# Kernel optimization log

Hardware: AMD Instinct MI355X
Metric: run time of the kernel (lower is better)

## Reference

```python
import jax, jax.numpy as jnp
import numpy as np

EPS = 1e-6

def rmsnorm(x, scale):
    return x * jax.lax.rsqrt(jnp.mean(x * x, axis=-1, keepdims=True) + EPS) * scale

def setup_inputs() -> dict:
    key = jax.random.key(0)
    ks = jax.random.split(key, 8)
    B1, B2 = 16, 64
    D, H, A = 8192, 1024, 2          # deter_size, hidden_size, action_size
    S, C, G = 32, 64, 8              # stoch_size, classes, blocks
    sc = 0.02                        # trunc-normal-ish init scale
    f32 = jnp.float32
    return dict(
        deter=jax.random.normal(ks[0], (B1, B2, D), f32),
        stoch=jax.random.normal(ks[1], (B1, B2, S, C), f32),
        action=jax.random.normal(ks[2], (B1, B2, A), f32),
        W1=(jax.random.normal(ks[3], (H, D), f32) * sc),
        b1=jnp.zeros((H,), f32),
        s1=jnp.ones((H,), f32),
        W2=(jax.random.normal(ks[4], (H, S * C), f32) * sc),
        b2=jnp.zeros((H,), f32),
        s2=jnp.ones((H,), f32),
        W3=(jax.random.normal(ks[5], (H, A), f32) * sc),
        b3=jnp.zeros((H,), f32),
        s3=jnp.ones((H,), f32),
        Wb1=(jax.random.normal(ks[6], (G, (3 * G * H + D) // G, D // G), f32) * sc),
        bb1=jnp.zeros((D,), f32),
        sb1=jnp.ones((D,), f32),
        Wb2=(jax.random.normal(ks[7], (G, D // G, 3 * D // G), f32) * sc),
        bb2=jnp.zeros((3 * D,), f32),
    )

def reference(deter, stoch, action, W1, b1, s1, W2, b2, s2, W3, b3, s3, Wb1, bb1, sb1, Wb2, bb2):
    batch_shape = deter.shape[:-1]
    D = deter.shape[-1]
    d = deter.reshape(-1, D)                       # (B, D)
    B = d.shape[0]
    G = Wb1.shape[0]
    H = W1.shape[0]
    s = stoch.reshape(B, -1)                       # (B, S*C)
    a = action.reshape(B, -1)                      # (B, A)
    a = a / jax.lax.stop_gradient(jnp.maximum(1.0, jnp.abs(a)))
    # three parallel Linear + RMSNorm + SiLU branches
    x1 = jax.nn.silu(rmsnorm(d @ W1.T + b1, s1))
    x2 = jax.nn.silu(rmsnorm(s @ W2.T + b2, s2))
    x3 = jax.nn.silu(rmsnorm(a @ W3.T + b3, s3))
    x = jnp.concatenate([x1, x2, x3], axis=-1)     # (B, 3H)
    x = jnp.broadcast_to(x[:, None, :], (B, G, 3 * H))
    x = jnp.concatenate([x, d.reshape(B, G, D // G)], axis=-1)  # (B, G, 3H + D/G)
    # block-diagonal grouped GEMM + RMSNorm + SiLU (dyn_layers=1)
    h = jnp.einsum('bgi,gio->bgo', x, Wb1).reshape(B, D) + bb1
    h = jax.nn.silu(rmsnorm(h, sb1))
    # final block-diagonal GEMM -> 3*D gate pre-activations
    y = jnp.einsum('bgi,gio->bgo', h.reshape(B, G, D // G), Wb2).reshape(B, 3 * D) + bb2
    r, c, u = jnp.split(y.reshape(B, G, -1), 3, axis=-1)        # each (B, G, D/G)
    reset = jax.nn.sigmoid(r.reshape(B, D))
    cand = jnp.tanh(reset * c.reshape(B, D))
    update = jax.nn.sigmoid(u.reshape(B, D) - 1.0)
    next_deter = update * cand + (1.0 - update) * d
    return next_deter.reshape(*batch_shape, D)
```

## Files before the change

### kernel.cpp

```cpp
#include <hip/hip_runtime.h>
#include <stdint.h>

typedef unsigned short ushort_t;
typedef __attribute__((ext_vector_type(8))) short bf16x8;
typedef __attribute__((ext_vector_type(4))) float f32x4;

#define EPS 1e-6f

__device__ __forceinline__ float b2f(ushort_t u) {
    union { uint32_t i; float f; } v; v.i = ((uint32_t)u) << 16; return v.f;
}
__device__ __forceinline__ ushort_t f2b(float f) {
    union { float f; uint32_t i; } v; v.f = f;
    uint32_t x = v.i;
    uint32_t r = (x + 0x7fffu + ((x >> 16) & 1u)) >> 16;
    return (ushort_t)r;
}

__device__ __forceinline__ void async_copy16(const void* g, void* l) {
    __builtin_amdgcn_global_load_lds(
        (const __attribute__((address_space(1))) uint32_t*)(uintptr_t)g,
        (__attribute__((address_space(3))) uint32_t*)(uintptr_t)l,
        16, 0, 0);
}

__global__ __launch_bounds__(256) void cast_f32_bf16_k(const float* __restrict__ src,
                                                       ushort_t* __restrict__ dst, int n4) {
    int i = blockIdx.x * 256 + threadIdx.x;
    if (i >= n4) return;
    float4 v = ((const float4*)src)[i];
    ushort4 o;
    o.x = f2b(v.x); o.y = f2b(v.y); o.z = f2b(v.z); o.w = f2b(v.w);
    ((ushort4*)dst)[i] = o;
}

__global__ __launch_bounds__(256) void zero_f32_k(float* __restrict__ dst, int n4) {
    int i = blockIdx.x * 256 + threadIdx.x;
    if (i >= n4) return;
    ((float4*)dst)[i] = make_float4(0.f, 0.f, 0.f, 0.f);
}

__global__ __launch_bounds__(256) void transpose_cast_k(const float* __restrict__ src,
                                                        ushort_t* __restrict__ dst,
                                                        int R, int C) {
    __shared__ float tile[32][33];
    int bat = blockIdx.z;
    int c0 = blockIdx.x * 32, r0 = blockIdx.y * 32;
    const float* s = src + (size_t)bat * R * C;
    ushort_t* d = dst + (size_t)bat * R * C;
    int tx = threadIdx.x, ty = threadIdx.y;
    float4 v = *(const float4*)&s[(size_t)(r0 + ty) * C + c0 + tx * 4];
    tile[ty][tx * 4 + 0] = v.x;
    tile[ty][tx * 4 + 1] = v.y;
    tile[ty][tx * 4 + 2] = v.z;
    tile[ty][tx * 4 + 3] = v.w;
    __syncthreads();
    ushort4 o;
    o.x = f2b(tile[tx * 4 + 0][ty]);
    o.y = f2b(tile[tx * 4 + 1][ty]);
    o.z = f2b(tile[tx * 4 + 2][ty]);
    o.w = f2b(tile[tx * 4 + 3][ty]);
    *(ushort4*)&d[(size_t)(c0 + ty) * R + r0 + tx * 4] = o;
}

template <int MODE, bool OUT_BF16, bool ATOMIC>
__global__ __launch_bounds__(256) void gemm_bt_k(
    const ushort_t* __restrict__ Aa, const ushort_t* __restrict__ Ab,
    const ushort_t* __restrict__ Bw,
    float* __restrict__ Cf, ushort_t* __restrict__ Cb,
    int lda, int ldb, int ldc, int Ksl, int k0base) {
    __shared__ __align__(16) ushort_t As[2][128 * 64];
    __shared__ __align__(16) ushort_t Bs[2][128 * 64];
    const int tid = threadIdx.x;

    const int nxy = gridDim.x * gridDim.y;
    const int flat = blockIdx.x + (blockIdx.y << 3);
    const int cpx = nxy >> 3;
    const int L = (flat & 7) * cpx + (flat >> 3);
    const int bm = L & 7, bn = L >> 3;
    const int bz = blockIdx.z;
    const int k0 = k0base + bz * Ksl;
    const int m0 = bm * 128, n0 = bn * 128;
    const int lane = tid & 63, w = tid >> 6;
    const int wm = (w & 1) * 64, wn = (w >> 1) * 64;

    f32x4 acc[4][4];
#pragma unroll
    for (int i = 0; i < 4; i++)
#pragma unroll
        for (int j = 0; j < 4; j++) acc[i][j] = (f32x4){0.f, 0.f, 0.f, 0.f};

    auto a_ptr = [&](int m, int kk) -> const ushort_t* {
        if (MODE == 0) {
            return Aa + (size_t)m * lda + kk;
        } else if (MODE == 1) {
            if (kk < 3072) return Aa + (size_t)m * 3072 + kk;
            int g = n0 >> 10;
            return Ab + (size_t)m * 8192 + g * 1024 + (kk - 3072);
        } else {
            int g = n0 / 3072;
            return Aa + (size_t)m * 8192 + g * 1024 + kk;
        }
    };

    const int srow = tid >> 3;
    const int sslot = tid & 7;
    const int gco = (sslot ^ (srow & 7)) << 3;
    const int lco = sslot << 3;

    auto stage = [&](int buf, int kk) {
#pragma unroll
        for (int p = 0; p < 4; ++p) {
            int r = (p << 5) + srow;
            async_copy16(a_ptr(m0 + r, kk + gco), &As[buf][r * 64 + lco]);
            async_copy16(Bw + (size_t)(n0 + r) * ldb + kk + gco, &Bs[buf][r * 64 + lco]);
        }
    };

    const int nt = Ksl >> 6;
    stage(0, k0);
    __syncthreads();

    const int qc = lane >> 4;
    const int rl = lane & 15;
    int cur = 0;

    for (int t = 0; t < nt; ++t) {
        if (t + 1 < nt) stage(cur ^ 1, k0 + ((t + 1) << 6));

#pragma unroll
        for (int h = 0; h < 2; ++h) {
            bf16x8 af[4], bfr[4];
#pragma unroll
            for (int i = 0; i < 4; i++) {
                int ra = wm + i * 16 + rl;
                int slot = ((h << 2) + qc) ^ (ra & 7);
                af[i] = *(const bf16x8*)&As[cur][ra * 64 + (slot << 3)];
            }
#pragma unroll
            for (int j = 0; j < 4; j++) {
                int rb = wn + j * 16 + rl;
                int slot = ((h << 2) + qc) ^ (rb & 7);
                bfr[j] = *(const bf16x8*)&Bs[cur][rb * 64 + (slot << 3)];
            }
#pragma unroll
            for (int i = 0; i < 4; i++)
#pragma unroll
                for (int j = 0; j < 4; j++)
                    acc[i][j] = __builtin_amdgcn_mfma_f32_16x16x32_bf16(af[i], bfr[j], acc[i][j], 0, 0, 0);
        }

        if (t + 1 < nt) {
            __syncthreads();
            cur ^= 1;
        }
    }

    const int cr = (lane >> 4) * 4, cc = lane & 15;
#pragma unroll
    for (int i = 0; i < 4; i++) {
#pragma unroll
        for (int j = 0; j < 4; j++) {
#pragma unroll
            for (int r = 0; r < 4; r++) {
                int row = m0 + wm + i * 16 + cr + r;
                int col = n0 + wn + j * 16 + cc;
                float v = acc[i][j][r];
                if (ATOMIC) {
                    atomicAdd(&Cf[(size_t)row * ldc + col], v);
                } else if (OUT_BF16) {
                    Cb[(size_t)row * ldc + col] = f2b(v);
                } else {
                    Cf[(size_t)row * ldc + col] = v;
                }
            }
        }
    }
}

__global__ __launch_bounds__(256) void branch3_k(const float* __restrict__ act,
                                                 const float* __restrict__ W3,
                                                 float* __restrict__ xpre) {
    int idx = blockIdx.x * 256 + threadIdx.x;
    int b = idx >> 10, h = idx & 1023;
    float a0 = act[b * 2 + 0], a1 = act[b * 2 + 1];
    a0 = a0 / fmaxf(1.f, fabsf(a0));
    a1 = a1 / fmaxf(1.f, fabsf(a1));
    float v = a0 * W3[h * 2 + 0] + a1 * W3[h * 2 + 1];
    xpre[(size_t)b * 3072 + 2048 + h] = v;
}

__global__ __launch_bounds__(256) void norm_silu_1024_k(
    const float* __restrict__ xpre,
    const float* __restrict__ b1, const float* __restrict__ s1,
    const float* __restrict__ b2, const float* __restrict__ s2,
    const float* __restrict__ b3, const float* __restrict__ s3,
    ushort_t* __restrict__ xbf) {
    int b = blockIdx.x, c = blockIdx.y, tid = threadIdx.x;
    const float* bias = (c == 0) ? b1 : (c == 1) ? b2 : b3;
    const float* scl  = (c == 0) ? s1 : (c == 1) ? s2 : s3;
    const float* src = xpre + (size_t)b * 3072 + c * 1024;
    float4 v = ((const float4*)src)[tid];
    float4 bb = ((const float4*)bias)[tid];
    v.x += bb.x; v.y += bb.y; v.z += bb.z; v.w += bb.w;
    float ss = v.x * v.x + v.y * v.y + v.z * v.z + v.w * v.w;
#pragma unroll
    for (int off = 32; off > 0; off >>= 1) ss += __shfl_down(ss, off, 64);
    __shared__ float wsum[4];
    int lane = tid & 63, wid = tid >> 6;
    if (lane == 0) wsum[wid] = ss;
    __syncthreads();
    float tot = wsum[0] + wsum[1] + wsum[2] + wsum[3];
    float rms = rsqrtf(tot * (1.0f / 1024.0f) + EPS);
    float4 sc = ((const float4*)scl)[tid];
    float o0 = v.x * rms * sc.x; o0 = o0 / (1.f + __expf(-o0));
    float o1 = v.y * rms * sc.y; o1 = o1 / (1.f + __expf(-o1));
    float o2 = v.z * rms * sc.z; o2 = o2 / (1.f + __expf(-o2));
    float o3 = v.w * rms * sc.w; o3 = o3 / (1.f + __expf(-o3));
    ushort4 o; o.x = f2b(o0); o.y = f2b(o1); o.z = f2b(o2); o.w = f2b(o3);
    ((ushort4*)(xbf + (size_t)b * 3072 + c * 1024))[tid] = o;
}

__global__ __launch_bounds__(256) void norm_silu_8192_k(const float* __restrict__ hpre,
                                                        const float* __restrict__ bb1,
                                                        const float* __restrict__ sb1,
                                                        ushort_t* __restrict__ hbf) {
    int b = blockIdx.x, tid = threadIdx.x;
    const float4* src = (const float4*)(hpre + (size_t)b * 8192);
    float4 v[8];
    float ss = 0.f;
#pragma unroll
    for (int k = 0; k < 8; k++) {
        float4 t = src[tid + k * 256];
        float4 bv = ((const float4*)bb1)[tid + k * 256];
        t.x += bv.x; t.y += bv.y; t.z += bv.z; t.w += bv.w;
        v[k] = t;
        ss += t.x * t.x + t.y * t.y + t.z * t.z + t.w * t.w;
    }
#pragma unroll
    for (int off = 32; off > 0; off >>= 1) ss += __shfl_down(ss, off, 64);
    __shared__ float wsum[4];
    int lane = tid & 63, wid = tid >> 6;
    if (lane == 0) wsum[wid] = ss;
    __syncthreads();
    float tot = wsum[0] + wsum[1] + wsum[2] + wsum[3];
    float rms = rsqrtf(tot * (1.0f / 8192.0f) + EPS);
    ushort_t* dst = hbf + (size_t)b * 8192;
#pragma unroll
    for (int k = 0; k < 8; k++) {
        float4 sv = ((const float4*)sb1)[tid + k * 256];
        float o0 = v[k].x * rms * sv.x; o0 = o0 / (1.f + __expf(-o0));
        float o1 = v[k].y * rms * sv.y; o1 = o1 / (1.f + __expf(-o1));
        float o2 = v[k].z * rms * sv.z; o2 = o2 / (1.f + __expf(-o2));
        float o3 = v[k].w * rms * sv.w; o3 = o3 / (1.f + __expf(-o3));
        ushort4 o; o.x = f2b(o0); o.y = f2b(o1); o.z = f2b(o2); o.w = f2b(o3);
        ((ushort4*)dst)[tid + k * 256] = o;
    }
}

__global__ __launch_bounds__(256) void gates_k(const ushort_t* __restrict__ y,
                                               const float* __restrict__ bb2,
                                               const float* __restrict__ deter,
                                               float* __restrict__ out) {
    int idx = blockIdx.x * 256 + threadIdx.x;
    int f = idx * 4;
    int b = f >> 13, d = f & 8191;
    int g = d >> 10, j = d & 1023;
    size_t ybase = (size_t)b * 24576 + g * 3072 + j;
    ushort4 rv = *(const ushort4*)(y + ybase);
    ushort4 cv = *(const ushort4*)(y + ybase + 1024);
    ushort4 uv = *(const ushort4*)(y + ybase + 2048);
    float4 bbr = *(const float4*)(bb2 + g * 3072 + j);
    float4 bbc = *(const float4*)(bb2 + g * 3072 + 1024 + j);
    float4 bbu = *(const float4*)(bb2 + g * 3072 + 2048 + j);
    float4 dv = *(const float4*)(deter + f);
    float rr[4] = {b2f(rv.x) + bbr.x, b2f(rv.y) + bbr.y, b2f(rv.z) + bbr.z, b2f(rv.w) + bbr.w};
    float cc[4] = {b2f(cv.x) + bbc.x, b2f(cv.y) + bbc.y, b2f(cv.z) + bbc.z, b2f(cv.w) + bbc.w};
    float uu[4] = {b2f(uv.x) + bbu.x, b2f(uv.y) + bbu.y, b2f(uv.z) + bbu.z, b2f(uv.w) + bbu.w};
    float dd[4] = {dv.x, dv.y, dv.z, dv.w};
    float oo[4];
#pragma unroll
    for (int t = 0; t < 4; t++) {
        float reset = 1.f / (1.f + __expf(-rr[t]));
        float cand = tanhf(reset * cc[t]);
        float upd = 1.f / (1.f + __expf(-(uu[t] - 1.f)));
        oo[t] = upd * cand + (1.f - upd) * dd[t];
    }
    float4 o; o.x = oo[0]; o.y = oo[1]; o.z = oo[2]; o.w = oo[3];
    *(float4*)(out + f) = o;
}

extern "C" void kernel_launch(void* const* d_in, const int* in_sizes, int n_in,
                              void* d_out, int out_size, void* d_ws, size_t ws_size,
                              hipStream_t stream) {
    const float* deter = (const float*)d_in[0];
    const float* stoch = (const float*)d_in[1];
    const float* action = (const float*)d_in[2];
    const float* W1 = (const float*)d_in[3];
    const float* b1 = (const float*)d_in[4];
    const float* s1 = (const float*)d_in[5];
    const float* W2 = (const float*)d_in[6];
    const float* b2 = (const float*)d_in[7];
    const float* s2 = (const float*)d_in[8];
    const float* W3 = (const float*)d_in[9];
    const float* b3 = (const float*)d_in[10];
    const float* s3 = (const float*)d_in[11];
    const float* Wb1 = (const float*)d_in[12];
    const float* bb1 = (const float*)d_in[13];
    const float* sb1 = (const float*)d_in[14];
    const float* Wb2 = (const float*)d_in[15];
    const float* bb2 = (const float*)d_in[16];
    float* out = (float*)d_out;

    char* ws = (char*)d_ws;
    ushort_t* dbf  = (ushort_t*)(ws + 0);
    ushort_t* sbf  = (ushort_t*)(ws + 16777216);
    ushort_t* W1bf = (ushort_t*)(ws + 20971520);
    ushort_t* W2bf = (ushort_t*)(ws + 37748736);
    ushort_t* Wb1T = (ushort_t*)(ws + 41943040);
    ushort_t* Wb2T = (ushort_t*)(ws + 109051904);
    float*    xpre = (float*)   (ws + 159383552);
    ushort_t* xbf  = (ushort_t*)(ws + 171966464);
    float*    hpre = (float*)   (ws + 178257920);
    ushort_t* hbf  = (ushort_t*)(ws + 211812352);
    ushort_t* ybf  = (ushort_t*)(ws + 228589568);

    cast_f32_bf16_k<<<8192, 256, 0, stream>>>(deter, dbf, 2097152);
    cast_f32_bf16_k<<<2048, 256, 0, stream>>>(stoch, sbf, 524288);
    cast_f32_bf16_k<<<8192, 256, 0, stream>>>(W1, W1bf, 2097152);
    cast_f32_bf16_k<<<2048, 256, 0, stream>>>(W2, W2bf, 524288);
    transpose_cast_k<<<dim3(32, 128, 8), dim3(8, 32), 0, stream>>>(Wb1, Wb1T, 4096, 1024);
    transpose_cast_k<<<dim3(96, 32, 8), dim3(8, 32), 0, stream>>>(Wb2, Wb2T, 1024, 3072);
    zero_f32_k<<<3072, 256, 0, stream>>>(xpre, 786432);

    gemm_bt_k<0, false, true><<<dim3(8, 8, 4), 256, 0, stream>>>(
        dbf, nullptr, W1bf, xpre, nullptr, 8192, 8192, 3072, 2048, 0);
    gemm_bt_k<0, false, true><<<dim3(8, 8, 2), 256, 0, stream>>>(
        sbf, nullptr, W2bf, xpre + 1024, nullptr, 2048, 2048, 3072, 1024, 0);
    branch3_k<<<4096, 256, 0, stream>>>(action, W3, xpre);

    norm_silu_1024_k<<<dim3(1024, 3), 256, 0, stream>>>(xpre, b1, s1, b2, s2, b3, s3, xbf);

    gemm_bt_k<1, false, false><<<dim3(8, 64, 1), 256, 0, stream>>>(
        xbf, dbf, Wb1T, hpre, nullptr, 0, 4096, 8192, 4096, 0);

    norm_silu_8192_k<<<1024, 256, 0, stream>>>(hpre, bb1, sb1, hbf);

    gemm_bt_k<2, true, false><<<dim3(8, 192, 1), 256, 0, stream>>>(
        hbf, nullptr, Wb2T, nullptr, ybf, 0, 1024, 24576, 1024, 0);

    gates_k<<<8192, 256, 0, stream>>>(ybf, bb2, deter, out);
}
```

Baseline: 634.0 us.

## Replace split-K atomics with partial buffers, fuse casts, and relax GEMM pipeline waits

The split-K GEMMs now write each K-slice to a separate region of a wider partial buffer instead of using atomicAdd. The norm kernel sums those partials, so the zeroing kernel and atomic contention go away. The four cast launches are merged into one kernel. The GEMM main loop swaps __syncthreads for explicit vmcnt waits plus s_barrier, so the next tile's async loads can stay in flight during compute. The partial buffer reuses the hpre workspace region, and the hand-written waitcnt counts must match the number of issued loads exactly.

```diff
diff --git a/kernel.cpp b/kernel.cpp
--- a/kernel.cpp
+++ b/kernel.cpp
@@ -24,20 +24,21 @@
         16, 0, 0);
 }
 
-__global__ __launch_bounds__(256) void cast_f32_bf16_k(const float* __restrict__ src,
-                                                       ushort_t* __restrict__ dst, int n4) {
-    int i = blockIdx.x * 256 + threadIdx.x;
-    if (i >= n4) return;
-    float4 v = ((const float4*)src)[i];
+__global__ __launch_bounds__(256) void cast4_k(
+    const float* __restrict__ s0, ushort_t* __restrict__ d0, int n0,
+    const float* __restrict__ s1, ushort_t* __restrict__ d1, int n1,
+    const float* __restrict__ s2, ushort_t* __restrict__ d2, int n2,
+    const float* __restrict__ s3, ushort_t* __restrict__ d3) {
+    int j = blockIdx.x * 256 + threadIdx.x;
+    const float* s; ushort_t* d;
+    if (j < n0) { s = s0; d = d0; }
+    else if ((j -= n0) < n1) { s = s1; d = d1; }
+    else if ((j -= n1) < n2) { s = s2; d = d2; }
+    else { j -= n2; s = s3; d = d3; }
+    float4 v = ((const float4*)s)[j];
     ushort4 o;
     o.x = f2b(v.x); o.y = f2b(v.y); o.z = f2b(v.z); o.w = f2b(v.w);
-    ((ushort4*)dst)[i] = o;
-}
-
-__global__ __launch_bounds__(256) void zero_f32_k(float* __restrict__ dst, int n4) {
-    int i = blockIdx.x * 256 + threadIdx.x;
-    if (i >= n4) return;
-    ((float4*)dst)[i] = make_float4(0.f, 0.f, 0.f, 0.f);
+    ((ushort4*)d)[j] = o;
 }
 
 __global__ __launch_bounds__(256) void transpose_cast_k(const float* __restrict__ src,
@@ -63,12 +64,12 @@
     *(ushort4*)&d[(size_t)(c0 + ty) * R + r0 + tx * 4] = o;
 }
 
-template <int MODE, bool OUT_BF16, bool ATOMIC>
+template <int MODE, bool OUT_BF16>
 __global__ __launch_bounds__(256) void gemm_bt_k(
     const ushort_t* __restrict__ Aa, const ushort_t* __restrict__ Ab,
     const ushort_t* __restrict__ Bw,
     float* __restrict__ Cf, ushort_t* __restrict__ Cb,
-    int lda, int ldb, int ldc, int Ksl, int k0base) {
+    int lda, int ldb, int ldc, int Ksl, int k0base, int czoff) {
     __shared__ __align__(16) ushort_t As[2][128 * 64];
     __shared__ __align__(16) ushort_t Bs[2][128 * 64];
     const int tid = threadIdx.x;
@@ -81,6 +82,7 @@
     const int bz = blockIdx.z;
     const int k0 = k0base + bz * Ksl;
     const int m0 = bm * 128, n0 = bn * 128;
+    const int cz = bz * czoff;
     const int lane = tid & 63, w = tid >> 6;
     const int wm = (w & 1) * 64, wn = (w >> 1) * 64;
 
@@ -119,14 +121,21 @@
 
     const int nt = Ksl >> 6;
     stage(0, k0);
-    __syncthreads();
+    __builtin_amdgcn_sched_barrier(0);
 
     const int qc = lane >> 4;
     const int rl = lane & 15;
     int cur = 0;
 
     for (int t = 0; t < nt; ++t) {
-        if (t + 1 < nt) stage(cur ^ 1, k0 + ((t + 1) << 6));
+        if (t + 1 < nt) {
+            stage(cur ^ 1, k0 + ((t + 1) << 6));
+            asm volatile("s_waitcnt vmcnt(8)" ::: "memory");
+        } else {
+            asm volatile("s_waitcnt vmcnt(0)" ::: "memory");
+        }
+        __builtin_amdgcn_s_barrier();
+        __builtin_amdgcn_sched_barrier(0);
 
 #pragma unroll
         for (int h = 0; h < 2; ++h) {
@@ -151,7 +160,9 @@
         }
 
         if (t + 1 < nt) {
-            __syncthreads();
+            __builtin_amdgcn_sched_barrier(0);
+            __builtin_amdgcn_s_barrier();
+            __builtin_amdgcn_sched_barrier(0);
             cur ^= 1;
         }
     }
@@ -164,11 +175,9 @@
 #pragma unroll
             for (int r = 0; r < 4; r++) {
                 int row = m0 + wm + i * 16 + cr + r;
-                int col = n0 + wn + j * 16 + cc;
+                int col = n0 + cz + wn + j * 16 + cc;
                 float v = acc[i][j][r];
-                if (ATOMIC) {
-                    atomicAdd(&Cf[(size_t)row * ldc + col], v);
-                } else if (OUT_BF16) {
+                if (OUT_BF16) {
                     Cb[(size_t)row * ldc + col] = f2b(v);
                 } else {
                     Cf[(size_t)row * ldc + col] = v;
@@ -180,18 +189,18 @@
 
 __global__ __launch_bounds__(256) void branch3_k(const float* __restrict__ act,
                                                  const float* __restrict__ W3,
-                                                 float* __restrict__ xpre) {
+                                                 float* __restrict__ xacc) {
     int idx = blockIdx.x * 256 + threadIdx.x;
     int b = idx >> 10, h = idx & 1023;
     float a0 = act[b * 2 + 0], a1 = act[b * 2 + 1];
     a0 = a0 / fmaxf(1.f, fabsf(a0));
     a1 = a1 / fmaxf(1.f, fabsf(a1));
     float v = a0 * W3[h * 2 + 0] + a1 * W3[h * 2 + 1];
-    xpre[(size_t)b * 3072 + 2048 + h] = v;
+    xacc[(size_t)b * 7168 + 6144 + h] = v;
 }
 
 __global__ __launch_bounds__(256) void norm_silu_1024_k(
-    const float* __restrict__ xpre,
+    const float* __restrict__ xacc,
     const float* __restrict__ b1, const float* __restrict__ s1,
     const float* __restrict__ b2, const float* __restrict__ s2,
     const float* __restrict__ b3, const float* __restrict__ s3,
@@ -199,8 +208,14 @@
     int b = blockIdx.x, c = blockIdx.y, tid = threadIdx.x;
     const float* bias = (c == 0) ? b1 : (c == 1) ? b2 : b3;
     const float* scl  = (c == 0) ? s1 : (c == 1) ? s2 : s3;
-    const float* src = xpre + (size_t)b * 3072 + c * 1024;
-    float4 v = ((const float4*)src)[tid];
+    const float* row = xacc + (size_t)b * 7168 + ((c == 0) ? 0 : (c == 1) ? 4096 : 6144);
+    const int np = (c == 0) ? 4 : (c == 1) ? 2 : 1;
+    float4 v = ((const float4*)row)[tid];
+#pragma unroll 4
+    for (int p = 1; p < np; ++p) {
+        float4 t = ((const float4*)(row + p * 1024))[tid];
+        v.x += t.x; v.y += t.y; v.z += t.z; v.w += t.w;
+    }
     float4 bb = ((const float4*)bias)[tid];
     v.x += bb.x; v.y += bb.y; v.z += bb.z; v.w += bb.w;
     float ss = v.x * v.x + v.y * v.y + v.z * v.z + v.w * v.w;
@@ -319,35 +334,34 @@
     ushort_t* W2bf = (ushort_t*)(ws + 37748736);
     ushort_t* Wb1T = (ushort_t*)(ws + 41943040);
     ushort_t* Wb2T = (ushort_t*)(ws + 109051904);
-    float*    xpre = (float*)   (ws + 159383552);
     ushort_t* xbf  = (ushort_t*)(ws + 171966464);
     float*    hpre = (float*)   (ws + 178257920);
     ushort_t* hbf  = (ushort_t*)(ws + 211812352);
     ushort_t* ybf  = (ushort_t*)(ws + 228589568);
-
-    cast_f32_bf16_k<<<8192, 256, 0, stream>>>(deter, dbf, 2097152);
-    cast_f32_bf16_k<<<2048, 256, 0, stream>>>(stoch, sbf, 524288);
-    cast_f32_bf16_k<<<8192, 256, 0, stream>>>(W1, W1bf, 2097152);
-    cast_f32_bf16_k<<<2048, 256, 0, stream>>>(W2, W2bf, 524288);
+    float*    xacc = hpre;
+
+    cast4_k<<<20480, 256, 0, stream>>>(deter, dbf, 2097152,
+                                       stoch, sbf, 524288,
+                                       W1, W1bf, 2097152,
+                                       W2, W2bf);
     transpose_cast_k<<<dim3(32, 128, 8), dim3(8, 32), 0, stream>>>(Wb1, Wb1T, 4096, 1024);
     transpose_cast_k<<<dim3(96, 32, 8), dim3(8, 32), 0, stream>>>(Wb2, Wb2T, 1024, 3072);
-    zero_f32_k<<<3072, 256, 0, stream>>>(xpre, 786432);
-
-    gemm_bt_k<0, false, true><<<dim3(8, 8, 4), 256, 0, stream>>>(
-        dbf, nullptr, W1bf, xpre, nullptr, 8192, 8192, 3072, 2048, 0);
-    gemm_bt_k<0, false, true><<<dim3(8, 8, 2), 256, 0, stream>>>(
-        sbf, nullptr, W2bf, xpre + 1024, nullptr, 2048, 2048, 3072, 1024, 0);
-    branch3_k<<<4096, 256, 0, stream>>>(action, W3, xpre);
-
-    norm_silu_1024_k<<<dim3(1024, 3), 256, 0, stream>>>(xpre, b1, s1, b2, s2, b3, s3, xbf);
-
-    gemm_bt_k<1, false, false><<<dim3(8, 64, 1), 256, 0, stream>>>(
-        xbf, dbf, Wb1T, hpre, nullptr, 0, 4096, 8192, 4096, 0);
+
+    gemm_bt_k<0, false><<<dim3(8, 8, 4), 256, 0, stream>>>(
+        dbf, nullptr, W1bf, xacc, nullptr, 8192, 8192, 7168, 2048, 0, 1024);
+    gemm_bt_k<0, false><<<dim3(8, 8, 2), 256, 0, stream>>>(
+        sbf, nullptr, W2bf, xacc + 4096, nullptr, 2048, 2048, 7168, 1024, 0, 1024);
+    branch3_k<<<4096, 256, 0, stream>>>(action, W3, xacc);
+
+    norm_silu_1024_k<<<dim3(1024, 3), 256, 0, stream>>>(xacc, b1, s1, b2, s2, b3, s3, xbf);
+
+    gemm_bt_k<1, false><<<dim3(8, 64, 1), 256, 0, stream>>>(
+        xbf, dbf, Wb1T, hpre, nullptr, 0, 4096, 8192, 4096, 0, 0);
 
     norm_silu_8192_k<<<1024, 256, 0, stream>>>(hpre, bb1, sb1, hbf);
 
-    gemm_bt_k<2, true, false><<<dim3(8, 192, 1), 256, 0, stream>>>(
-        hbf, nullptr, Wb2T, nullptr, ybf, 0, 1024, 24576, 1024, 0);
+    gemm_bt_k<2, true><<<dim3(8, 192, 1), 256, 0, stream>>>(
+        hbf, nullptr, Wb2T, nullptr, ybf, 0, 1024, 24576, 1024, 0, 0);
 
     gates_k<<<8192, 256, 0, stream>>>(ybf, bb2, deter, out);
 }
```

After: 595.3 us. 1.07x faster.
